# Optimization experiments

Hardware: AMD Instinct MI355X
Metric: run time of the kernel (lower is better)

The kernel has to match this reference:

```python
import jax, jax.numpy as jnp
import numpy as np

D = 768   # embedding_dimensions (richness) — hardcoded in source
H = 3     # heads — hardcoded in source


def setup_inputs() -> dict:
    key = jax.random.key(0)
    ks = jax.random.split(key, 12)
    s = 1.0 / np.sqrt(D)
    s3 = 1.0 / np.sqrt(H * D)
    return {
        "x": jax.random.normal(ks[0], (4, 2048, D), dtype=jnp.float32),
        # QKV projections: Linear(D, D*H), stored as (in, out)
        "Wq": jax.random.uniform(ks[1], (D, D * H), jnp.float32, -s, s),
        "bq": jax.random.uniform(ks[2], (D * H,), jnp.float32, -s, s),
        "Wk": jax.random.uniform(ks[3], (D, D * H), jnp.float32, -s, s),
        "bk": jax.random.uniform(ks[4], (D * H,), jnp.float32, -s, s),
        "Wv": jax.random.uniform(ks[5], (D, D * H), jnp.float32, -s, s),
        "bv": jax.random.uniform(ks[6], (D * H,), jnp.float32, -s, s),
        # final projection: Linear(H*D, D)
        "Wo": jax.random.uniform(ks[7], (H * D, D), jnp.float32, -s3, s3),
        "bo": jax.random.uniform(ks[8], (D,), jnp.float32, -s3, s3),
        # FFN: Linear(D, D) + LeakyReLU
        "Wf": jax.random.uniform(ks[9], (D, D), jnp.float32, -s, s),
        "bf": jax.random.uniform(ks[10], (D,), jnp.float32, -s, s),
    }


def reference(x, Wq, bq, Wk, bk, Wv, bv, Wo, bo, Wf, bf):
    B, S, _ = x.shape
    # QKV: [B,S,H*D] -> [B,H,S,D]  (head dim == full D, as in source)
    q = (x @ Wq + bq).reshape(B, S, H, D).transpose(0, 2, 1, 3)
    k = (x @ Wk + bk).reshape(B, S, H, D).transpose(0, 2, 1, 3)
    v = (x @ Wv + bv).reshape(B, S, H, D).transpose(0, 2, 1, 3)
    # unscaled attention scores (source applies no 1/sqrt(d))
    scores = jnp.einsum('bhqd,bhkd->bhqk', q, k)
    # faithful masking: tril of the scores themselves, fill zeros with -99999
    masked = jnp.where(jnp.tril(scores) == 0, jnp.float32(-99999.0), scores)
    attn = jax.nn.softmax(masked, axis=-1)
    o = jnp.einsum('bhqk,bhkd->bhqd', attn, v)
    o = o.transpose(0, 2, 1, 3).reshape(B, S, H * D)
    a = o @ Wo + bo
    # "normalisation": subtract global mean over the whole tensor
    n = a - jnp.mean(a)
    y = n + x  # residual
    return jax.nn.leaky_relu(y @ Wf + bf, negative_slope=0.01)
```

## Files before the change

### kernel.cpp

```cpp
#include <hip/hip_runtime.h>
#include <hip/hip_bf16.h>

typedef __attribute__((ext_vector_type(8))) __bf16 bf16x8;
typedef __attribute__((ext_vector_type(4))) float f32x4;
typedef unsigned short u16;

#define DEV static __device__ __forceinline__

#define BAR() asm volatile("s_barrier" ::: "memory")
#define LGKM0() asm volatile("s_waitcnt lgkmcnt(0)" ::: "memory")
#define VMCNT3() asm volatile("s_waitcnt vmcnt(3)" ::: "memory")
#define VMCNT2() asm volatile("s_waitcnt vmcnt(2)" ::: "memory")
#define VMCNT0() asm volatile("s_waitcnt vmcnt(0)" ::: "memory")

DEV void load_lds16(const void* g, void* l) {
  __builtin_amdgcn_global_load_lds(
      (const __attribute__((address_space(1))) unsigned int*)g,
      (__attribute__((address_space(3))) unsigned int*)l, 16, 0, 0);
}

DEV u16 bf16bits(float v) {
  __hip_bfloat16 h = __float2bfloat16(v);
  return __builtin_bit_cast(u16, h);
}

DEV float bf2f(u16 u) {
  return __builtin_bit_cast(float, (unsigned)u << 16);
}

DEV bf16x8 rdfrag(const u16* region, int row, int ks, int l) {
  const int cb = (((ks << 6) | ((l >> 4) << 4)) ^ ((l & 7) << 4));
  return *(const bf16x8*)((const char*)region + row * 128 + cb);
}

DEV bf16x8 rdfrag32(const u16* region, int row, int l) {
  const int cb = (((l >> 4) ^ ((row >> 1) & 3)) << 4);
  return *(const bf16x8*)((const char*)region + row * 64 + cb);
}

struct OffN { unsigned long long a[12], b[12], c[12]; };

enum { G128_SC = 0, G128_PV = 1, G128_PLAIN = 2, G128_LEAKY = 3 };

__global__ __launch_bounds__(512, 1) void k_qkv256(
    const u16* __restrict__ A, const u16* __restrict__ B,
    const float* __restrict__ bias, u16* __restrict__ C, u16* __restrict__ Vt)
{
  int flat = blockIdx.y * 27 + blockIdx.x;
  flat = (flat & 7) * 108 + (flat >> 3);
  const int n0 = (flat % 27) * 256, m0 = (flat / 27) * 256;
  const int lda = 768, ldb = 768, nkt = 12;

  __shared__ u16 smem[65536];

  const int tid = threadIdx.x;
  const int l = tid & 63;
  const int wid = tid >> 6;
  const int wm = wid >> 1, wn = wid & 1;

  const int r0s = wid * 16 + (l >> 3);
  const int ces = ((l & 7) ^ (l >> 3)) << 3;
  const size_t aR0 = (size_t)(m0 + r0s) * lda + ces;
  const size_t aR1 = aR0 + (size_t)8 * lda;
  const size_t bR0 = (size_t)(n0 + r0s) * ldb + ces;
  const size_t bR1 = bR0 + (size_t)8 * ldb;
  const size_t hA = (size_t)128 * lda, hB = (size_t)128 * ldb;
  const int dst0 = wid * 1024 + l * 8, dst1 = dst0 + 512;
  u16* As0 = smem;
  u16* Bs0 = smem + 32768;

#define STAGE_A(bf, h, kkv) do {                                 \
    u16* Lp = As0 + (bf) * 16384 + (h) * 8192;                   \
    load_lds16(A + aR0 + ((h) ? hA : 0) + (kkv), Lp + dst0);     \
    load_lds16(A + aR1 + ((h) ? hA : 0) + (kkv), Lp + dst1);     \
  } while (0)
#define STAGE_B(bf, h, kkv) do {                                 \
    u16* Lp = Bs0 + (bf) * 16384 + (h) * 8192;                   \
    load_lds16(B + bR0 + ((h) ? hB : 0) + (kkv), Lp + dst0);     \
    load_lds16(B + bR1 + ((h) ? hB : 0) + (kkv), Lp + dst1);     \
  } while (0)

  f32x4 acc[2][2][2][4] = {};
  bf16x8 af[2][2], bA[4][2], bB[4][2];

#define MFMA16(QM, QN, BARR)                                                  \
    __builtin_amdgcn_s_setprio(1);                                            \
    _Pragma("unroll") for (int ks = 0; ks < 2; ks++)                          \
      _Pragma("unroll") for (int fm = 0; fm < 2; fm++)                        \
        _Pragma("unroll") for (int fn = 0; fn < 4; fn++)                      \
          acc[QM][QN][fm][fn] = __builtin_amdgcn_mfma_f32_16x16x32_bf16(      \
              af[fm][ks], BARR[fn][ks], acc[QM][QN][fm][fn], 0, 0, 0);        \
    __builtin_amdgcn_s_setprio(0);

#define RD_A(half)                                                            \
    _Pragma("unroll") for (int fm = 0; fm < 2; fm++)                          \
      _Pragma("unroll") for (int ks = 0; ks < 2; ks++)                        \
        af[fm][ks] = rdfrag(half, wm * 32 + fm * 16 + (l & 15), ks, l);
#define RD_B(dstv, half)                                                      \
    _Pragma("unroll") for (int fn = 0; fn < 4; fn++)                          \
      _Pragma("unroll") for (int ks = 0; ks < 2; ks++)                        \
        dstv[fn][ks] = rdfrag(half, wn * 64 + fn * 16 + (l & 15), ks, l);

  STAGE_A(0, 0, 0); STAGE_B(0, 0, 0); STAGE_B(0, 1, 0); STAGE_A(0, 1, 0);
  STAGE_A(1, 0, 64); STAGE_B(1, 0, 64); STAGE_B(1, 1, 64);
  VMCNT3();
  BAR();

  for (int t = 0; t < nkt; ++t) {
    const int cur = t & 1, nxt = cur ^ 1;
    const int kk1 = (t + 1) << 6, kk2 = (t + 2) << 6;
    const bool s1 = (t + 1 < nkt), s2 = (t + 2 < nkt);
    RD_A(As0 + cur * 16384);
    RD_B(bA, Bs0 + cur * 16384);
    if (s1) STAGE_A(nxt, 1, kk1);
    BAR(); LGKM0();
    MFMA16(0, 0, bA);
    BAR();
    RD_B(bB, Bs0 + cur * 16384 + 8192);
    if (s2) STAGE_A(cur, 0, kk2);
    BAR(); LGKM0();
    MFMA16(0, 1, bB);
    BAR();
    RD_A(As0 + cur * 16384 + 8192);
    if (s2) STAGE_B(cur, 0, kk2);
    BAR(); LGKM0();
    MFMA16(1, 1, bB);
    BAR();
    if (s2) STAGE_B(cur, 1, kk2);
    BAR();
    MFMA16(1, 0, bA);
    if (s2) { VMCNT3(); } else { VMCNT0(); }
    BAR();
  }
#undef RD_A
#undef RD_B
#undef MFMA16
#undef STAGE_A
#undef STAGE_B

  __syncthreads();
  const int sel = n0 >= 4608 ? 2 : (n0 >= 2304 ? 1 : 0);
  const int r0c = (l >> 4) << 2;
  if (sel == 2) {
#pragma unroll
    for (int Qm = 0; Qm < 2; Qm++)
#pragma unroll
      for (int Qn = 0; Qn < 2; Qn++)
#pragma unroll
        for (int fn = 0; fn < 4; fn++) {
          const int coll = Qn * 128 + wn * 64 + fn * 16 + (l & 15);
          const float bv = bias[n0 + coll];
#pragma unroll
          for (int fm = 0; fm < 2; fm++)
#pragma unroll
            for (int r = 0; r < 4; r++) {
              const int rowl = Qm * 128 + wm * 32 + fm * 16 + r0c + r;
              smem[coll * 256 + ((((rowl >> 3) ^ (coll & 7)) << 3) | (rowl & 7))] =
                  bf16bits(acc[Qm][Qn][fm][fn][r] + bv);
            }
        }
    __syncthreads();
    const int n0v = n0 - 4608;
    const int h = n0v / 768, d0l = n0v % 768;
    const int b = m0 >> 11, sbase = m0 & 2047;
    u16* Cb = Vt + ((size_t)(b * 3 + h) * 768 + d0l) * 2048 + sbase;
#pragma unroll
    for (int j = 0; j < 16; j++) {
      const int dr = j * 16 + (tid >> 5);
      const int c8 = tid & 31;
      bf16x8 v = *(const bf16x8*)&smem[dr * 256 + ((c8 ^ (dr & 7)) << 3)];
      *(bf16x8*)&Cb[(size_t)dr * 2048 + c8 * 8] = v;
    }
  } else {
#pragma unroll
    for (int Qm = 0; Qm < 2; Qm++)
#pragma unroll
      for (int Qn = 0; Qn < 2; Qn++)
#pragma unroll
        for (int fn = 0; fn < 4; fn++) {
          const int coll = Qn * 128 + wn * 64 + fn * 16 + (l & 15);
          const float bv = bias[n0 + coll];
#pragma unroll
          for (int fm = 0; fm < 2; fm++)
#pragma unroll
            for (int r = 0; r < 4; r++) {
              const int rowl = Qm * 128 + wm * 32 + fm * 16 + r0c + r;
              smem[rowl * 256 + (coll ^ (((rowl >> 2) & 3) << 4))] =
                  bf16bits(acc[Qm][Qn][fm][fn][r] + bv);
            }
        }
    __syncthreads();
    u16* Cb = C + (size_t)sel * (8192ull * 2304) + (n0 - sel * 2304);
#pragma unroll
    for (int j = 0; j < 16; j++) {
      const int rowl = j * 16 + (tid >> 5);
      const int c = (tid & 31) * 8;
      bf16x8 v = *(const bf16x8*)&smem[rowl * 256 + (c ^ (((rowl >> 2) & 3) << 4))];
      *(bf16x8*)&Cb[(size_t)(m0 + rowl) * 2304 + c] = v;
    }
  }
}

template<int MODE>
__global__ __launch_bounds__(512, 6) void k_g128(
    const u16* __restrict__ Abase, const u16* __restrict__ Bbase,
    const float* __restrict__ bias, void* __restrict__ Cbase,
    float* __restrict__ part,
    long lda, long ldb, long ldc, int K, OffN off)
{
  int m0, n0, z, r = 0, rb = 0, nkt, arow0, brow0, bx = 0;
  const u16 *A, *B;
  if (MODE == G128_SC) {
    r = blockIdx.y; z = blockIdx.z; bx = blockIdx.x;
    rb = r >> 1;
    if (bx > (r | 1)) return;
    m0 = r * 128; n0 = bx * 128;
    nkt = K >> 5;
    A = Abase + off.a[z]; B = Bbase + off.b[z];
    arow0 = m0; brow0 = n0;
  } else if (MODE == G128_PV) {
    r = 15 - (int)blockIdx.y;
    rb = r >> 1;
    z = blockIdx.x / 6;
    m0 = r * 128; n0 = (blockIdx.x % 6) * 128;
    nkt = (rb + 1) * 8;
    lda = (long)(rb + 1) * 256;
    A = Abase + off.a[z] + (size_t)32768 * rb * (rb + 1);
    B = Bbase + off.b[z];
    arow0 = (r & 1) * 128; brow0 = n0;
  } else {
    z = 0;
    m0 = blockIdx.y * 128; n0 = blockIdx.x * 128;
    nkt = K >> 5;
    A = Abase; B = Bbase;
    arow0 = m0; brow0 = n0;
  }

  __shared__ u16 smem[24576];

  const int tid = threadIdx.x;
  const int l = tid & 63;
  const int wid = tid >> 6;
  const int wm = wid & 1;
  const int wn = wid >> 1;

  const int ces = (((tid & 3) ^ ((tid >> 3) & 3)) << 3);
  const u16* aS = A + (size_t)(arow0 + (tid >> 2)) * lda + ces;
  const u16* bS = B + (size_t)(brow0 + (tid >> 2)) * ldb + ces;
  const int t8 = tid * 8;

#define STG(buf, kkv) do {                    \
    u16* Lp = smem + (buf) * 8192;            \
    load_lds16(aS + (kkv), Lp + t8);          \
    load_lds16(bS + (kkv), Lp + 4096 + t8);   \
  } while (0)

  f32x4 acc[4][2] = {};
  bf16x8 af[4], bf[2];

  STG(0, 0);
  STG(1, 32);
  VMCNT2();
  BAR();

  for (int t = 0; t < nkt; ++t) {
    const u16* Ar = smem + (t % 3) * 8192;
    const u16* Br = Ar + 4096;
#pragma unroll
    for (int fm = 0; fm < 4; fm++)
      af[fm] = rdfrag32(Ar, wm * 64 + fm * 16 + (l & 15), l);
#pragma unroll
    for (int fn = 0; fn < 2; fn++)
      bf[fn] = rdfrag32(Br, wn * 32 + fn * 16 + (l & 15), l);
    const bool s2 = (t + 2 < nkt);
    if (s2) STG((t + 2) % 3, (t + 2) << 5);
    LGKM0();
    __builtin_amdgcn_s_setprio(1);
#pragma unroll
    for (int fm = 0; fm < 4; fm++)
#pragma unroll
      for (int fn = 0; fn < 2; fn++)
        acc[fm][fn] = __builtin_amdgcn_mfma_f32_16x16x32_bf16(
            af[fm], bf[fn], acc[fm][fn], 0, 0, 0);
    __builtin_amdgcn_s_setprio(0);
    if (s2) { VMCNT2(); } else if (t + 1 < nkt) { VMCNT0(); }
    BAR();
  }
#undef STG

  const int r0c = (l >> 4) << 2;
  if (MODE == G128_SC) {
    float mx4[4][4], s4[4][4];
#pragma unroll
    for (int fm = 0; fm < 4; fm++)
#pragma unroll
      for (int rr = 0; rr < 4; rr++) {
        const int gi = m0 + wm * 64 + fm * 16 + r0c + rr;
        float mv = -1e30f;
#pragma unroll
        for (int fn = 0; fn < 2; fn++) {
          const int gc = n0 + wn * 32 + fn * 16 + (l & 15);
          float v = (gc <= gi) ? acc[fm][fn][rr] : -1e30f;
          acc[fm][fn][rr] = v;
          mv = fmaxf(mv, v);
        }
        mx4[fm][rr] = mv;
      }
#pragma unroll
    for (int o = 1; o < 16; o <<= 1)
#pragma unroll
      for (int fm = 0; fm < 4; fm++)
#pragma unroll
        for (int rr = 0; rr < 4; rr++)
          mx4[fm][rr] = fmaxf(mx4[fm][rr], __shfl_xor(mx4[fm][rr], o, 64));
    float* redm = (float*)smem;
    float* reds = redm + 512;
#pragma unroll
    for (int fm = 0; fm < 4; fm++)
#pragma unroll
      for (int rr = 0; rr < 4; rr++)
        if ((l & 15) == fm * 4 + rr)
          redm[(wm * 64 + fm * 16 + r0c + rr) * 4 + wn] = mx4[fm][rr];
    __syncthreads();
#pragma unroll
    for (int fm = 0; fm < 4; fm++)
#pragma unroll
      for (int rr = 0; rr < 4; rr++) {
        const int rowl = wm * 64 + fm * 16 + r0c + rr;
        f32x4 rm = *(const f32x4*)&redm[rowl * 4];
        const float tm = fmaxf(fmaxf(rm[0], rm[1]), fmaxf(rm[2], rm[3]));
        float ss = 0.f;
#pragma unroll
        for (int fn = 0; fn < 2; fn++) {
          const float v = acc[fm][fn][rr];
          const float e = (v > -1e29f) ? __expf(v - tm) : 0.f;
          acc[fm][fn][rr] = e;
          ss += e;
        }
        s4[fm][rr] = ss;
      }
#pragma unroll
    for (int o = 1; o < 16; o <<= 1)
#pragma unroll
      for (int fm = 0; fm < 4; fm++)
#pragma unroll
        for (int rr = 0; rr < 4; rr++)
          s4[fm][rr] += __shfl_xor(s4[fm][rr], o, 64);
#pragma unroll
    for (int fm = 0; fm < 4; fm++)
#pragma unroll
      for (int rr = 0; rr < 4; rr++)
        if ((l & 15) == fm * 4 + rr)
          reds[(wm * 64 + fm * 16 + r0c + rr) * 4 + wn] = s4[fm][rr];
    __syncthreads();
    if (tid < 128) {
      f32x4 rm = *(const f32x4*)&redm[tid * 4];
      f32x4 rs = *(const f32x4*)&reds[tid * 4];
      float2 pw;
      pw.x = fmaxf(fmaxf(rm[0], rm[1]), fmaxf(rm[2], rm[3]));
      pw.y = rs[0] + rs[1] + rs[2] + rs[3];
      ((float2*)part)[((size_t)z * 16 + bx) * 2048 + m0 + tid] = pw;
    }
    __syncthreads();
#pragma unroll
    for (int fn = 0; fn < 2; fn++) {
      const int coll = wn * 32 + fn * 16 + (l & 15);
#pragma unroll
      for (int fm = 0; fm < 4; fm++)
#pragma unroll
        for (int rr = 0; rr < 4; rr++) {
          const int rowl = wm * 64 + fm * 16 + r0c + rr;
          smem[rowl * 128 + (coll ^ (((rowl >> 2) & 3) << 4))] =
              bf16bits(acc[fm][fn][rr]);
        }
    }
    __syncthreads();
    u16* Cb = (u16*)Cbase + off.c[z] + (size_t)32768 * rb * (rb + 1);
    const int W = (rb + 1) << 8;
    const int pr0 = (r & 1) * 128;
#pragma unroll
    for (int j = 0; j < 4; j++) {
      const int rowl = j * 32 + (tid >> 4);
      const int c = tid & 15;
      bf16x8 v = *(const bf16x8*)&smem[rowl * 128 + ((c ^ (((rowl >> 2) & 3) << 1)) << 3)];
      *(bf16x8*)&Cb[(size_t)(pr0 + rowl) * W + n0 + c * 8] = v;
    }
  } else if (MODE == G128_PV) {
    __syncthreads();
#pragma unroll
    for (int fn = 0; fn < 2; fn++) {
      const int coll = wn * 32 + fn * 16 + (l & 15);
#pragma unroll
      for (int fm = 0; fm < 4; fm++)
#pragma unroll
        for (int rr = 0; rr < 4; rr++) {
          const int rowl = wm * 64 + fm * 16 + r0c + rr;
          smem[rowl * 128 + (coll ^ (((rowl >> 2) & 3) << 4))] =
              bf16bits(acc[fm][fn][rr]);
        }
    }
    __syncthreads();
    u16* Cb = (u16*)Cbase + off.c[z] + n0;
#pragma unroll
    for (int j = 0; j < 4; j++) {
      const int rowl = j * 32 + (tid >> 4);
      const int c = tid & 15;
      bf16x8 v = *(const bf16x8*)&smem[rowl * 128 + ((c ^ (((rowl >> 2) & 3) << 1)) << 3)];
      *(bf16x8*)&Cb[(size_t)(m0 + rowl) * 2304 + c * 8] = v;
    }
  } else {
#pragma unroll
    for (int fn = 0; fn < 2; fn++) {
      const int col = n0 + wn * 32 + fn * 16 + (l & 15);
      const float bv = bias[col];
#pragma unroll
      for (int fm = 0; fm < 4; fm++)
#pragma unroll
        for (int rr = 0; rr < 4; rr++) {
          const int rowl = wm * 64 + fm * 16 + r0c + rr;
          float v = acc[fm][fn][rr] + bv;
          if (MODE == G128_LEAKY) v = v > 0.f ? v : 0.01f * v;
          ((float*)Cbase)[(size_t)(m0 + rowl) * ldc + col] = v;
        }
    }
  }
}

__global__ __launch_bounds__(256) void k_cast_x(const float* __restrict__ in,
                                                u16* __restrict__ out) {
  const size_t i = ((size_t)blockIdx.x * 256 + threadIdx.x) * 4;
  float4 v = *(const float4*)&in[i];
  ushort4 o;
  o.x = bf16bits(v.x); o.y = bf16bits(v.y); o.z = bf16bits(v.z); o.w = bf16bits(v.w);
  *(ushort4*)&out[i] = o;
}

__global__ __launch_bounds__(256) void k_wt(const float* __restrict__ in,
                                            u16* __restrict__ out, int R, int C) {
  __shared__ float tile[32][33];
  const int c0 = blockIdx.x * 32, r0 = blockIdx.y * 32;
  const int tx = threadIdx.x, ty = threadIdx.y;
#pragma unroll
  for (int k = 0; k < 4; k++)
    tile[ty + 8 * k][tx] = in[(size_t)(r0 + ty + 8 * k) * C + c0 + tx];
  __syncthreads();
#pragma unroll
  for (int k = 0; k < 4; k++)
    out[(size_t)(c0 + ty + 8 * k) * R + r0 + tx] = bf16bits(tile[tx][ty + 8 * k]);
}

__global__ __launch_bounds__(256) void k_bias_concat(const float* __restrict__ bq,
                                                     const float* __restrict__ bk,
                                                     const float* __restrict__ bv,
                                                     float* __restrict__ out) {
  const int i = blockIdx.x * 256 + threadIdx.x;
  if (i < 2304) out[i] = bq[i];
  else if (i < 4608) out[i] = bk[i - 2304];
  else if (i < 6912) out[i] = bv[i - 4608];
}

__global__ __launch_bounds__(256) void k_rescale(u16* __restrict__ P,
                                                 const float* __restrict__ part) {
  const int w = threadIdx.x >> 6, l = threadIdx.x & 63;
  const int gi = blockIdx.x * 4 + w;
  const int z = blockIdx.y;
  const int rb = gi >> 8;
  const int W = (rb + 1) << 8;
  const int nt = (gi >> 7) + 1;
  const float2* pp = (const float2*)part + (size_t)z * 16 * 2048 + gi;
  float m = -1e30f;
  for (int t = 0; t < nt; t++) m = fmaxf(m, pp[(size_t)t * 2048].x);
  float den = 0.f;
  for (int t = 0; t < nt; t++) {
    float2 q = pp[(size_t)t * 2048];
    den += q.y * __expf(q.x - m);
  }
  const float inv = 1.f / den;
  u16* Prow = P + (size_t)z * 2359296 + (size_t)32768 * rb * (rb + 1) +
              (size_t)(gi & 255) * W;
  for (int t = 0; t < nt; t++) {
    const float ft = __expf(pp[(size_t)t * 2048].x - m) * inv;
    unsigned v = *(const unsigned*)&Prow[t * 128 + l * 2];
    const float lo = bf2f((u16)(v & 0xffff)) * ft;
    const float hi = bf2f((u16)(v >> 16)) * ft;
    unsigned o = (unsigned)bf16bits(lo) | ((unsigned)bf16bits(hi) << 16);
    *(unsigned*)&Prow[t * 128 + l * 2] = o;
  }
}

__global__ __launch_bounds__(256) void k_red1(const float* __restrict__ a,
                                              float* __restrict__ part) {
  float s = 0.f;
  for (size_t idx = (size_t)blockIdx.x * 256 + threadIdx.x; idx < 6291456ull; idx += 2048ull * 256)
    s += a[idx];
#pragma unroll
  for (int o = 32; o >= 1; o >>= 1) s += __shfl_xor(s, o, 64);
  __shared__ float r[4];
  const int t = threadIdx.x, w = t >> 6;
  if ((t & 63) == 0) r[w] = s;
  __syncthreads();
  if (t == 0) part[blockIdx.x] = r[0] + r[1] + r[2] + r[3];
}

__global__ __launch_bounds__(256) void k_red2(const float* __restrict__ part,
                                              float* __restrict__ mean) {
  const int t = threadIdx.x;
  float s = 0.f;
  for (int i = t; i < 2048; i += 256) s += part[i];
#pragma unroll
  for (int o = 32; o >= 1; o >>= 1) s += __shfl_xor(s, o, 64);
  __shared__ float r[4];
  const int w = t >> 6;
  if ((t & 63) == 0) r[w] = s;
  __syncthreads();
  if (t == 0) mean[0] = (r[0] + r[1] + r[2] + r[3]) * (1.f / 6291456.f);
}

__global__ __launch_bounds__(256) void k_residual(const float* __restrict__ a,
                                                  const float* __restrict__ x,
                                                  const float* __restrict__ meanp,
                                                  u16* __restrict__ yb) {
  const float mean = meanp[0];
  const size_t i = ((size_t)blockIdx.x * 256 + threadIdx.x) * 4;
  float4 av = *(const float4*)&a[i];
  float4 xv = *(const float4*)&x[i];
  ushort4 o;
  o.x = bf16bits(av.x - mean + xv.x);
  o.y = bf16bits(av.y - mean + xv.y);
  o.z = bf16bits(av.z - mean + xv.z);
  o.w = bf16bits(av.w - mean + xv.w);
  *(ushort4*)&yb[i] = o;
}

extern "C" void kernel_launch(void* const* d_in, const int* in_sizes, int n_in,
                              void* d_out, int out_size, void* d_ws, size_t ws_size,
                              hipStream_t stream) {
  const float* x   = (const float*)d_in[0];
  const float* Wq  = (const float*)d_in[1];
  const float* bq  = (const float*)d_in[2];
  const float* Wk  = (const float*)d_in[3];
  const float* bk  = (const float*)d_in[4];
  const float* Wv  = (const float*)d_in[5];
  const float* bv  = (const float*)d_in[6];
  const float* Wo  = (const float*)d_in[7];
  const float* bo  = (const float*)d_in[8];
  const float* Wf  = (const float*)d_in[9];
  const float* bfb = (const float*)d_in[10];

  char* ws = (char*)d_ws;
  const size_t MSZ    = 37748736;
  const size_t o_Wqkvt = 0;
  const size_t o_Wot  = 10616832;
  const size_t o_Wft  = o_Wot + 3538944;
  const size_t o_bqkv = o_Wft + 1179648;
  const size_t o_prt  = o_bqkv + 32768;
  const size_t o_mn   = o_prt + 8192;
  const size_t o_part = o_mn + 256;
  const size_t o_xb   = o_part + 3145728;
  const size_t o_Q    = o_xb + 12582912;
  const size_t o_K    = o_Q + MSZ;
  const size_t o_Vt   = o_K + MSZ;
  const size_t o_P    = o_Vt + MSZ;
  const size_t o_end  = o_P + 56623104;
  if (ws_size < o_end) return;

  const size_t o_O  = o_Q;
  const size_t o_a  = o_K;
  const size_t o_yb = o_xb;

  OffN z0{};
  dim3 b32(32, 8);

  k_cast_x<<<6144, 256, 0, stream>>>(x, (u16*)(ws + o_xb));
  k_wt<<<dim3(72, 24), b32, 0, stream>>>(Wq, (u16*)(ws + o_Wqkvt), 768, 2304);
  k_wt<<<dim3(72, 24), b32, 0, stream>>>(Wk, (u16*)(ws + o_Wqkvt) + 2304 * 768, 768, 2304);
  k_wt<<<dim3(72, 24), b32, 0, stream>>>(Wv, (u16*)(ws + o_Wqkvt) + 2 * 2304 * 768, 768, 2304);
  k_wt<<<dim3(24, 72), b32, 0, stream>>>(Wo, (u16*)(ws + o_Wot), 2304, 768);
  k_wt<<<dim3(24, 24), b32, 0, stream>>>(Wf, (u16*)(ws + o_Wft), 768, 768);
  k_bias_concat<<<27, 256, 0, stream>>>(bq, bk, bv, (float*)(ws + o_bqkv));

  k_qkv256<<<dim3(27, 32), 512, 0, stream>>>(
      (const u16*)(ws + o_xb), (const u16*)(ws + o_Wqkvt),
      (const float*)(ws + o_bqkv), (u16*)(ws + o_Q), (u16*)(ws + o_Vt));

  OffN so{}, po{};
  for (int zz = 0; zz < 12; zz++) {
    const int b = zz / 3, h = zz % 3;
    so.a[zz] = (size_t)b * 2048 * 2304 + (size_t)h * 768;
    so.b[zz] = so.a[zz];
    so.c[zz] = (size_t)zz * 2359296;
    po.a[zz] = so.c[zz];
    po.b[zz] = (size_t)zz * 768 * 2048;
    po.c[zz] = so.a[zz];
  }
  k_g128<G128_SC><<<dim3(16, 16, 12), 512, 0, stream>>>(
      (const u16*)(ws + o_Q), (const u16*)(ws + o_K), nullptr, ws + o_P,
      (float*)(ws + o_part), 2304, 2304, 0, 768, so);
  k_rescale<<<dim3(512, 12), 256, 0, stream>>>((u16*)(ws + o_P),
                                               (const float*)(ws + o_part));
  k_g128<G128_PV><<<dim3(72, 16), 512, 0, stream>>>(
      (const u16*)(ws + o_P), (const u16*)(ws + o_Vt), nullptr, ws + o_O,
      nullptr, 0, 2048, 0, 0, po);

  k_g128<G128_PLAIN><<<dim3(6, 64), 512, 0, stream>>>(
      (const u16*)(ws + o_O), (const u16*)(ws + o_Wot), bo, ws + o_a,
      nullptr, 2304, 2304, 768, 2304, z0);

  k_red1<<<2048, 256, 0, stream>>>((const float*)(ws + o_a), (float*)(ws + o_prt));
  k_red2<<<1, 256, 0, stream>>>((const float*)(ws + o_prt), (float*)(ws + o_mn));
  k_residual<<<6144, 256, 0, stream>>>((const float*)(ws + o_a), x,
                                       (const float*)(ws + o_mn), (u16*)(ws + o_yb));

  k_g128<G128_LEAKY><<<dim3(6, 64), 512, 0, stream>>>(
      (const u16*)(ws + o_yb), (const u16*)(ws + o_Wft), bfb, d_out,
      nullptr, 768, 768, 768, 768, z0);
}
```

Measured before the change: 450.0 us.

## Deepen k_g128 pipeline to five LDS stages with double-buffered register fragments

The 128x128 GEMM kernel moves from a 3-stage to a 5-stage LDS ring, keeping four K-tiles of global loads in flight. It also ping-pongs two register fragment sets so LDS reads for the next tile overlap the MFMAs of the current one. LDS use grows to 80KB per block and launch bounds drop occupancy from 6 to 4 blocks. This trades occupancy for latency hiding, and the loop is unrolled by 2, which assumes nkt is even.

```diff
diff --git a/kernel.cpp b/kernel.cpp
--- a/kernel.cpp
+++ b/kernel.cpp
@@ -9,6 +9,7 @@
 
 #define BAR() asm volatile("s_barrier" ::: "memory")
 #define LGKM0() asm volatile("s_waitcnt lgkmcnt(0)" ::: "memory")
+#define VMCNT4() asm volatile("s_waitcnt vmcnt(4)" ::: "memory")
 #define VMCNT3() asm volatile("s_waitcnt vmcnt(3)" ::: "memory")
 #define VMCNT2() asm volatile("s_waitcnt vmcnt(2)" ::: "memory")
 #define VMCNT0() asm volatile("s_waitcnt vmcnt(0)" ::: "memory")
@@ -202,7 +203,7 @@
 }
 
 template<int MODE>
-__global__ __launch_bounds__(512, 6) void k_g128(
+__global__ __launch_bounds__(512, 4) void k_g128(
     const u16* __restrict__ Abase, const u16* __restrict__ Bbase,
     const float* __restrict__ bias, void* __restrict__ Cbase,
     float* __restrict__ part,
@@ -236,7 +237,7 @@
     arow0 = m0; brow0 = n0;
   }
 
-  __shared__ u16 smem[24576];
+  __shared__ u16 smem[40960];
 
   const int tid = threadIdx.x;
   const int l = tid & 63;
@@ -255,38 +256,53 @@
     load_lds16(bS + (kkv), Lp + 4096 + t8);   \
   } while (0)
 
+#define RDF(afv, bfv, base) do {                                      \
+    const u16* Ar = (base);                                           \
+    const u16* Br = (base) + 4096;                                    \
+    _Pragma("unroll") for (int fm = 0; fm < 4; fm++)                  \
+      afv[fm] = rdfrag32(Ar, wm * 64 + fm * 16 + (l & 15), l);        \
+    _Pragma("unroll") for (int fn = 0; fn < 2; fn++)                  \
+      bfv[fn] = rdfrag32(Br, wn * 32 + fn * 16 + (l & 15), l);        \
+  } while (0)
+
+#define MM(afv, bfv)                                                  \
+    __builtin_amdgcn_s_setprio(1);                                    \
+    _Pragma("unroll") for (int fm = 0; fm < 4; fm++)                  \
+      _Pragma("unroll") for (int fn = 0; fn < 2; fn++)                \
+        acc[fm][fn] = __builtin_amdgcn_mfma_f32_16x16x32_bf16(        \
+            afv[fm], bfv[fn], acc[fm][fn], 0, 0, 0);                  \
+    __builtin_amdgcn_s_setprio(0);
+
+#define WAITK(u) do {                                   \
+    if ((u) + 4 < nkt) { VMCNT4(); }                    \
+    else if ((u) + 3 < nkt) { VMCNT2(); }               \
+    else if ((u) + 2 < nkt) { VMCNT0(); }               \
+  } while (0)
+
   f32x4 acc[4][2] = {};
-  bf16x8 af[4], bf[2];
-
-  STG(0, 0);
-  STG(1, 32);
-  VMCNT2();
+  bf16x8 afA[4], bfA[2], afB[4], bfB[2];
+
+  STG(0, 0); STG(1, 32); STG(2, 64); STG(3, 96);
+  VMCNT4();
   BAR();
-
-  for (int t = 0; t < nkt; ++t) {
-    const u16* Ar = smem + (t % 3) * 8192;
-    const u16* Br = Ar + 4096;
-#pragma unroll
-    for (int fm = 0; fm < 4; fm++)
-      af[fm] = rdfrag32(Ar, wm * 64 + fm * 16 + (l & 15), l);
-#pragma unroll
-    for (int fn = 0; fn < 2; fn++)
-      bf[fn] = rdfrag32(Br, wn * 32 + fn * 16 + (l & 15), l);
-    const bool s2 = (t + 2 < nkt);
-    if (s2) STG((t + 2) % 3, (t + 2) << 5);
-    LGKM0();
-    __builtin_amdgcn_s_setprio(1);
-#pragma unroll
-    for (int fm = 0; fm < 4; fm++)
-#pragma unroll
-      for (int fn = 0; fn < 2; fn++)
-        acc[fm][fn] = __builtin_amdgcn_mfma_f32_16x16x32_bf16(
-            af[fm], bf[fn], acc[fm][fn], 0, 0, 0);
-    __builtin_amdgcn_s_setprio(0);
-    if (s2) { VMCNT2(); } else if (t + 1 < nkt) { VMCNT0(); }
+  RDF(afA, bfA, smem);
+
+  for (int t = 0; t < nkt; t += 2) {
+    RDF(afB, bfB, smem + ((t + 1) % 5) * 8192);
+    if (t + 4 < nkt) STG((t + 4) % 5, (t + 4) << 5);
+    MM(afA, bfA);
+    WAITK(t);
     BAR();
+    if (t + 2 < nkt) RDF(afA, bfA, smem + ((t + 2) % 5) * 8192);
+    if (t + 5 < nkt) STG((t + 5) % 5, (t + 5) << 5);
+    MM(afB, bfB);
+    WAITK(t + 1);
+    BAR();
   }
 #undef STG
+#undef RDF
+#undef MM
+#undef WAITK
 
   const int r0c = (l >> 4) << 2;
   if (MODE == G128_SC) {
```

Result: no change. 454.3 us (+1.0%).
